# Kernel tuning notes

Measured on AMD Instinct MI355X. Metric: run time of the kernel, lower is better.

## Reference

```python
import jax, jax.numpy as jnp
import numpy as np

B, H = 1024, 256
HP = H // 2  # hyperparams_dim
W_SCALE = 0.08  # kaiming-uniform-like magnitude to keep tanh unsaturated


def setup_inputs() -> dict:
    key = jax.random.key(0)
    ks = jax.random.split(key, 8)
    return {
        "h_0": jax.random.normal(ks[0], (B, 1, H), dtype=jnp.float32),
        "h_t": jax.random.normal(ks[1], (B, 1, H), dtype=jnp.float32),
        "msg": jax.random.normal(ks[2], (B, 1, H), dtype=jnp.float32),
        "c": jax.random.uniform(ks[3], (1,), dtype=jnp.float32),
        "fc1_w": jax.random.normal(ks[4], (HP, H), dtype=jnp.float32) * W_SCALE,
        "fc2_w": jax.random.normal(ks[5], (HP, HP), dtype=jnp.float32) * W_SCALE,
        "fc3_w": jax.random.normal(ks[6], (HP, HP), dtype=jnp.float32) * W_SCALE,
        "fc4_w": jax.random.normal(ks[7], (2 * H * H, HP), dtype=jnp.float32) * W_SCALE,
    }


def reference(h_0, h_t, msg, c, fc1_w, fc2_w, fc3_w, fc4_w):
    # torch code clamps self.c into [0, 1] before use
    cc = jnp.clip(c, 0.0, 1.0)
    h = cc * h_0 + (1.0 - cc) * h_t                     # [B, 1, H]
    x = jnp.tanh(jnp.einsum('bsh,ph->bsp', h, fc1_w))    # [B, 1, HP]
    x = jnp.tanh(jnp.einsum('bsp,qp->bsq', x, fc2_w))    # [B, 1, HP]
    x = jnp.tanh(jnp.einsum('bsq,rq->bsr', x, fc3_w))    # [B, 1, HP]
    f4 = jnp.einsum('bsr,wr->bsw', x, fc4_w)             # [B, 1, 2*H*H]
    g1 = f4[..., : H * H].reshape(-1, H, H)              # [B, H, H]
    g2 = f4[..., H * H :].reshape(-1, H, H)              # [B, H, H]
    # F.linear(msg[i], g) == msg[i] @ g.T, batched over B
    g1_out = jnp.tanh(jnp.einsum('bsh,bkh->bsk', msg, g1))  # [B, 1, H]
    out = jnp.einsum('bsk,bok->bso', g1_out, g2)             # [B, 1, H]
    return out
```

## Files before the change

kernel.cpp:

```cpp
#include <hip/hip_runtime.h>
#include <hip/hip_bf16.h>

#define HDIM 256
#define HPDIM 128

typedef short bf8 __attribute__((ext_vector_type(8)));
typedef float f32x4 __attribute__((ext_vector_type(4)));

__device__ inline unsigned pkbf2(float a, float b) {
  float2 f; f.x = a; f.y = b;
  __hip_bfloat162 h = __float22bfloat162_rn(f);
  unsigned u; __builtin_memcpy(&u, &h, 4); return u;
}
__device__ inline unsigned short bfbits(float v) {
  __hip_bfloat16 h = __float2bfloat16(v);
  unsigned short u; __builtin_memcpy(&u, &h, 2); return u;
}
__device__ inline uint4 pack8u(float4 a, float4 b) {
  uint4 r;
  r.x = pkbf2(a.x, a.y); r.y = pkbf2(a.z, a.w);
  r.z = pkbf2(b.x, b.y); r.w = pkbf2(b.z, b.w);
  return r;
}
__device__ inline float fast_tanh(float x) {
  float t = __expf(2.0f * x);
  return 1.0f - 2.0f * __builtin_amdgcn_rcpf(t + 1.0f);
}
__device__ inline bf8 wfrag(const float* __restrict__ s) {
  float4 a = *(const float4*)s, b = *(const float4*)(s + 4);
  uint4 u = pack8u(a, b);
  bf8 r; __builtin_memcpy(&r, &u, 16); return r;
}

typedef const __attribute__((address_space(1))) unsigned int* gas_ptr;
typedef __attribute__((address_space(3))) unsigned int* las_ptr;
__device__ inline void gld_lds16(const void* g, void* l) {
  __builtin_amdgcn_global_load_lds((gas_ptr)g, (las_ptr)l, 16, 0, 0);
}

__global__ __launch_bounds__(256) void k_prep(
    const float* __restrict__ h0, const float* __restrict__ htv,
    const float* __restrict__ cp,
    const float* __restrict__ w1, const float* __restrict__ w2,
    const float* __restrict__ w3, const float* __restrict__ msg,
    const float* __restrict__ fc4,
    short* __restrict__ x3f, float* __restrict__ msgTT,
    short* __restrict__ fc4f) {
  const int t = threadIdx.x;
  const int bx = blockIdx.x;

  if (bx >= 80) {
    const int tile = bx - 80;
    const float* srcp = fc4 + (size_t)tile * (64 * 128);
    char* dstp = (char*)fc4f + (size_t)tile * (64 * 256);
    #pragma unroll
    for (int it = 0; it < 4; ++it) {
      int cid = it * 256 + t;
      int rl = cid >> 4, c = cid & 15;
      const float* s = srcp + rl * 128 + c * 8;
      float4 a = *(const float4*)s, b = *(const float4*)(s + 4);
      *(uint4*)(dstp + rl * 256 + ((c ^ (rl & 7)) << 4)) = pack8u(a, b);
    }
    return;
  }

  if (bx >= 64) {
    const int b0 = (bx - 64) * 64;
    #pragma unroll
    for (int it = 0; it < 16; ++it) {
      int u = it * 256 + t;
      int bl = u & 63, g = u >> 6;
      float4 v = *(const float4*)(msg + (size_t)(b0 + bl) * HDIM + g * 4);
      *(float4*)(msgTT + (size_t)g * 4096 + (b0 + bl) * 4) = v;
    }
    return;
  }

  __shared__ char hbuf[8192];
  __shared__ char xa[4096];
  __shared__ char xb[4096];
  const int wave = t >> 6, lane = t & 63;
  const int r16 = lane & 15, quad = lane >> 4;
  const int b0 = bx * 16;
  const float cc = fminf(fmaxf(cp[0], 0.f), 1.f);

  #pragma unroll
  for (int it = 0; it < 2; ++it) {
    int flat = it * 2048 + t * 8;
    int row = flat >> 8, col = flat & 255, kb = col >> 3;
    int gi = (b0 + row) * HDIM + col;
    float4 a = *(const float4*)(h0 + gi);
    float4 b = *(const float4*)(htv + gi);
    float4 va, vb;
    va.x = cc*a.x + (1.f-cc)*b.x; va.y = cc*a.y + (1.f-cc)*b.y;
    va.z = cc*a.z + (1.f-cc)*b.z; va.w = cc*a.w + (1.f-cc)*b.w;
    a = *(const float4*)(h0 + gi + 4); b = *(const float4*)(htv + gi + 4);
    vb.x = cc*a.x + (1.f-cc)*b.x; vb.y = cc*a.y + (1.f-cc)*b.y;
    vb.z = cc*a.z + (1.f-cc)*b.z; vb.w = cc*a.w + (1.f-cc)*b.w;
    *(uint4*)(hbuf + row*512 + ((kb ^ (row & 7)) << 4)) = pack8u(va, vb);
  }
  __syncthreads();

  {
    f32x4 acc[2] = {};
    #pragma unroll
    for (int ks = 0; ks < 8; ++ks) {
      bf8 af = *(bf8*)(hbuf + r16*512 + (((ks*4 + quad) ^ (r16 & 7)) << 4));
      #pragma unroll
      for (int nt = 0; nt < 2; ++nt) {
        bf8 bw_ = wfrag(w1 + ((wave*2 + nt)*16 + r16) * 256 + ks*32 + quad*8);
        acc[nt] = __builtin_amdgcn_mfma_f32_16x16x32_bf16(af, bw_, acc[nt], 0, 0, 0);
      }
    }
    #pragma unroll
    for (int nt = 0; nt < 2; ++nt)
      #pragma unroll
      for (int i = 0; i < 4; ++i) {
        int row = quad*4 + i, col = wave*32 + nt*16 + r16;
        *(unsigned short*)(xa + row*256 + (((col >> 3) ^ (row & 7)) << 4) + ((col & 7) << 1))
            = bfbits(fast_tanh(acc[nt][i]));
      }
  }
  __syncthreads();
  {
    f32x4 acc[2] = {};
    #pragma unroll
    for (int ks = 0; ks < 4; ++ks) {
      bf8 af = *(bf8*)(xa + r16*256 + (((ks*4 + quad) ^ (r16 & 7)) << 4));
      #pragma unroll
      for (int nt = 0; nt < 2; ++nt) {
        bf8 bw_ = wfrag(w2 + ((wave*2 + nt)*16 + r16) * 128 + ks*32 + quad*8);
        acc[nt] = __builtin_amdgcn_mfma_f32_16x16x32_bf16(af, bw_, acc[nt], 0, 0, 0);
      }
    }
    #pragma unroll
    for (int nt = 0; nt < 2; ++nt)
      #pragma unroll
      for (int i = 0; i < 4; ++i) {
        int row = quad*4 + i, col = wave*32 + nt*16 + r16;
        *(unsigned short*)(xb + row*256 + (((col >> 3) ^ (row & 7)) << 4) + ((col & 7) << 1))
            = bfbits(fast_tanh(acc[nt][i]));
      }
  }
  __syncthreads();
  {
    f32x4 acc[2] = {};
    #pragma unroll
    for (int ks = 0; ks < 4; ++ks) {
      bf8 af = *(bf8*)(xb + r16*256 + (((ks*4 + quad) ^ (r16 & 7)) << 4));
      #pragma unroll
      for (int nt = 0; nt < 2; ++nt) {
        bf8 bw_ = wfrag(w3 + ((wave*2 + nt)*16 + r16) * 128 + ks*32 + quad*8);
        acc[nt] = __builtin_amdgcn_mfma_f32_16x16x32_bf16(af, bw_, acc[nt], 0, 0, 0);
      }
    }
    #pragma unroll
    for (int nt = 0; nt < 2; ++nt)
      #pragma unroll
      for (int i = 0; i < 4; ++i) {
        int row = quad*4 + i, col = wave*32 + nt*16 + r16;
        *(unsigned short*)(xa + row*256 + (((col >> 3) ^ (row & 7)) << 4) + ((col & 7) << 1))
            = bfbits(fast_tanh(acc[nt][i]));
      }
  }
  __syncthreads();
  {
    int ks = t >> 6, l = t & 63, q2 = l >> 4, rr = l & 15;
    uint4 d = *(uint4*)(xa + rr*256 + (((ks*4 + q2) ^ (rr & 7)) << 4));
    *(uint4*)(x3f + (size_t)((bx*4 + ks)*64 + l)*8) = d;
  }
}

template<int PHASE>
__global__ __launch_bounds__(256, 3) void k_hyper(
    const short* __restrict__ x3f, const float* __restrict__ wTT,
    const short* __restrict__ fc4f, float* __restrict__ outp) {
  __shared__ char lds[2 * 16384];
  const int bxs = blockIdx.x;
  const int kcol = ((bxs & 7) << 5) | (bxs >> 3);
  const int t = threadIdx.x, wave = t >> 6, lane = t & 63;
  const int r16 = lane & 15, quad = lane >> 4;
  const int bw = blockIdx.y * 256 + wave * 64;

  bf8 xf[4][4];
  #pragma unroll
  for (int nt = 0; nt < 4; ++nt)
    #pragma unroll
    for (int ks = 0; ks < 4; ++ks)
      xf[nt][ks] = *(const bf8*)(x3f +
          (size_t)(((blockIdx.y*16 + wave*4 + nt)*4 + ks)*64 + lane)*8);

  const char* src = (const char*)fc4f +
      ((size_t)(PHASE ? 65536 : 0) + (size_t)kcol * 256) * 256;

  #pragma unroll
  for (int it = 0; it < 4; ++it)
    gld_lds16(src + it*4096 + t*16, (char*)lds + it*4096 + t*16);
  __syncthreads();

  float gacc[4] = {0.f, 0.f, 0.f, 0.f};
  const float* wbase = wTT + (size_t)quad * 4096 + (bw + r16) * 4;

  #pragma unroll 1
  for (int q = 0; q < 4; ++q) {
    char* buf = (char*)lds + (q & 1) * 16384;
    float4 wv[4];
    #pragma unroll
    for (int nt = 0; nt < 4; ++nt)
      wv[nt] = *(const float4*)(wbase + (size_t)(q * 16) * 4096 + nt * 64);
    if (q < 3) {
      char* nbuf = (char*)lds + ((q + 1) & 1) * 16384;
      const char* nsrc = src + (q + 1) * 16384;
      #pragma unroll
      for (int it = 0; it < 4; ++it)
        gld_lds16(nsrc + it*4096 + t*16, nbuf + it*4096 + t*16);
    }
    #pragma unroll
    for (int htl = 0; htl < 4; ++htl) {
      if (htl > 0) {
        #pragma unroll
        for (int nt = 0; nt < 4; ++nt)
          wv[nt] = *(const float4*)(wbase + (size_t)(q*16 + htl*4) * 4096 + nt * 64);
      }
      const int row = htl * 16 + r16;
      bf8 af[4];
      #pragma unroll
      for (int ks = 0; ks < 4; ++ks)
        af[ks] = *(bf8*)(buf + row*256 + (((ks*4 + quad) ^ (row & 7)) << 4));
      #pragma unroll
      for (int nt = 0; nt < 4; ++nt) {
        f32x4 acc = {};
        #pragma unroll
        for (int ks = 0; ks < 4; ++ks)
          acc = __builtin_amdgcn_mfma_f32_16x16x32_bf16(af[ks], xf[nt][ks], acc, 0, 0, 0);
        gacc[nt] += acc[0]*wv[nt].x + acc[1]*wv[nt].y + acc[2]*wv[nt].z + acc[3]*wv[nt].w;
      }
    }
    __syncthreads();
  }

  #pragma unroll
  for (int nt = 0; nt < 4; ++nt) {
    float v = gacc[nt];
    v += __shfl_xor(v, 16);
    v += __shfl_xor(v, 32);
    if (quad == 0) {
      int b = bw + nt*16 + r16;
      if (PHASE == 0) outp[(size_t)(kcol >> 2)*4096 + b*4 + (kcol & 3)] = fast_tanh(v);
      else            outp[b*HDIM + kcol] = v;
    }
  }
}

extern "C" void kernel_launch(void* const* d_in, const int* in_sizes, int n_in,
                              void* d_out, int out_size, void* d_ws, size_t ws_size,
                              hipStream_t stream) {
  const float* h0  = (const float*)d_in[0];
  const float* htt = (const float*)d_in[1];
  const float* msg = (const float*)d_in[2];
  const float* c   = (const float*)d_in[3];
  const float* w1  = (const float*)d_in[4];
  const float* w2  = (const float*)d_in[5];
  const float* w3  = (const float*)d_in[6];
  const float* w4  = (const float*)d_in[7];
  float* out = (float*)d_out;

  short* x3f  = (short*)d_ws;
  float* g1TT = (float*)((char*)d_ws + 262144);
  float* msgTT= (float*)((char*)d_ws + 262144 + 1048576);
  short* fc4f = (short*)((char*)d_ws + 262144 + 2097152);

  k_prep<<<dim3(2128), dim3(256), 0, stream>>>(h0, htt, c, w1, w2, w3, msg, w4,
                                               x3f, msgTT, fc4f);
  k_hyper<0><<<dim3(256, 4), dim3(256), 0, stream>>>(x3f, msgTT, fc4f, g1TT);
  k_hyper<1><<<dim3(256, 4), dim3(256), 0, stream>>>(x3f, g1TT, fc4f, out);
}
```

Before: 178.6 us.

## Convert fc4 to bf16 inside hyper kernels and load full tile into LDS

Removes the separate fp32-to-bf16 conversion pass over fc4 in k_prep. Each k_hyper block now reads its 256-row fc4 slice directly as fp32, converts it and stores the whole 64KB swizzled tile in LDS at once, replacing the double-buffered global_load_lds pipeline. Blocks grow to 512 threads covering 512 batch rows, so each fc4 slice is read by half as many blocks. The inner loop is unrolled with ping-pong register prefetch of LDS fragments and weights. The cost is that each phase now reads the fp32 weight twice from HBM and gets lower occupancy because of the 64KB LDS per block.

```diff
diff --git a/kernel.cpp b/kernel.cpp
--- a/kernel.cpp
+++ b/kernel.cpp
@@ -32,37 +32,14 @@
   bf8 r; __builtin_memcpy(&r, &u, 16); return r;
 }
 
-typedef const __attribute__((address_space(1))) unsigned int* gas_ptr;
-typedef __attribute__((address_space(3))) unsigned int* las_ptr;
-__device__ inline void gld_lds16(const void* g, void* l) {
-  __builtin_amdgcn_global_load_lds((gas_ptr)g, (las_ptr)l, 16, 0, 0);
-}
-
 __global__ __launch_bounds__(256) void k_prep(
     const float* __restrict__ h0, const float* __restrict__ htv,
     const float* __restrict__ cp,
     const float* __restrict__ w1, const float* __restrict__ w2,
     const float* __restrict__ w3, const float* __restrict__ msg,
-    const float* __restrict__ fc4,
-    short* __restrict__ x3f, float* __restrict__ msgTT,
-    short* __restrict__ fc4f) {
+    short* __restrict__ x3f, float* __restrict__ msgTT) {
   const int t = threadIdx.x;
   const int bx = blockIdx.x;
-
-  if (bx >= 80) {
-    const int tile = bx - 80;
-    const float* srcp = fc4 + (size_t)tile * (64 * 128);
-    char* dstp = (char*)fc4f + (size_t)tile * (64 * 256);
-    #pragma unroll
-    for (int it = 0; it < 4; ++it) {
-      int cid = it * 256 + t;
-      int rl = cid >> 4, c = cid & 15;
-      const float* s = srcp + rl * 128 + c * 8;
-      float4 a = *(const float4*)s, b = *(const float4*)(s + 4);
-      *(uint4*)(dstp + rl * 256 + ((c ^ (rl & 7)) << 4)) = pack8u(a, b);
-    }
-    return;
-  }
 
   if (bx >= 64) {
     const int b0 = (bx - 64) * 64;
@@ -172,15 +149,15 @@
 }
 
 template<int PHASE>
-__global__ __launch_bounds__(256, 3) void k_hyper(
+__global__ __launch_bounds__(512) void k_hyper(
     const short* __restrict__ x3f, const float* __restrict__ wTT,
-    const short* __restrict__ fc4f, float* __restrict__ outp) {
-  __shared__ char lds[2 * 16384];
+    const float* __restrict__ fc4, float* __restrict__ outp) {
+  __shared__ char lds[65536];
   const int bxs = blockIdx.x;
   const int kcol = ((bxs & 7) << 5) | (bxs >> 3);
   const int t = threadIdx.x, wave = t >> 6, lane = t & 63;
   const int r16 = lane & 15, quad = lane >> 4;
-  const int bw = blockIdx.y * 256 + wave * 64;
+  const int bw = blockIdx.y * 512 + wave * 64;
 
   bf8 xf[4][4];
   #pragma unroll
@@ -188,55 +165,68 @@
     #pragma unroll
     for (int ks = 0; ks < 4; ++ks)
       xf[nt][ks] = *(const bf8*)(x3f +
-          (size_t)(((blockIdx.y*16 + wave*4 + nt)*4 + ks)*64 + lane)*8);
-
-  const char* src = (const char*)fc4f +
-      ((size_t)(PHASE ? 65536 : 0) + (size_t)kcol * 256) * 256;
-
-  #pragma unroll
-  for (int it = 0; it < 4; ++it)
-    gld_lds16(src + it*4096 + t*16, (char*)lds + it*4096 + t*16);
+          (size_t)((((blockIdx.y*8 + wave)*4 + nt)*4 + ks)*64 + lane)*8);
+
+  const float* src = fc4 + ((size_t)(PHASE ? 65536 : 0) + (size_t)kcol * 256) * HPDIM;
+  #pragma unroll
+  for (int it = 0; it < 8; ++it) {
+    int cidx = it * 512 + t;
+    int row = cidx >> 4, kb = cidx & 15;
+    const float* s = src + cidx * 8;
+    float4 a = *(const float4*)s, b = *(const float4*)(s + 4);
+    *(uint4*)(lds + row*256 + ((kb ^ (row & 7)) << 4)) = pack8u(a, b);
+  }
   __syncthreads();
 
   float gacc[4] = {0.f, 0.f, 0.f, 0.f};
   const float* wbase = wTT + (size_t)quad * 4096 + (bw + r16) * 4;
 
-  #pragma unroll 1
-  for (int q = 0; q < 4; ++q) {
-    char* buf = (char*)lds + (q & 1) * 16384;
-    float4 wv[4];
-    #pragma unroll
-    for (int nt = 0; nt < 4; ++nt)
-      wv[nt] = *(const float4*)(wbase + (size_t)(q * 16) * 4096 + nt * 64);
-    if (q < 3) {
-      char* nbuf = (char*)lds + ((q + 1) & 1) * 16384;
-      const char* nsrc = src + (q + 1) * 16384;
-      #pragma unroll
-      for (int it = 0; it < 4; ++it)
-        gld_lds16(nsrc + it*4096 + t*16, nbuf + it*4096 + t*16);
-    }
-    #pragma unroll
-    for (int htl = 0; htl < 4; ++htl) {
-      if (htl > 0) {
-        #pragma unroll
-        for (int nt = 0; nt < 4; ++nt)
-          wv[nt] = *(const float4*)(wbase + (size_t)(q*16 + htl*4) * 4096 + nt * 64);
-      }
-      const int row = htl * 16 + r16;
-      bf8 af[4];
-      #pragma unroll
-      for (int ks = 0; ks < 4; ++ks)
-        af[ks] = *(bf8*)(buf + row*256 + (((ks*4 + quad) ^ (row & 7)) << 4));
-      #pragma unroll
-      for (int nt = 0; nt < 4; ++nt) {
-        f32x4 acc = {};
-        #pragma unroll
-        for (int ks = 0; ks < 4; ++ks)
-          acc = __builtin_amdgcn_mfma_f32_16x16x32_bf16(af[ks], xf[nt][ks], acc, 0, 0, 0);
-        gacc[nt] += acc[0]*wv[nt].x + acc[1]*wv[nt].y + acc[2]*wv[nt].z + acc[3]*wv[nt].w;
-      }
-    }
-    __syncthreads();
+  float4 wvA[4], wvB[4];
+  bf8 afA[4], afB[4];
+  #pragma unroll
+  for (int nt = 0; nt < 4; ++nt) wvA[nt] = *(const float4*)(wbase + nt * 64);
+  #pragma unroll
+  for (int ks = 0; ks < 4; ++ks)
+    afA[ks] = *(bf8*)(lds + r16*256 + (((ks*4 + quad) ^ (r16 & 7)) << 4));
+
+  #pragma unroll
+  for (int hp = 0; hp < 8; ++hp) {
+    const int hgB = hp*2 + 1;
+    {
+      const int row = hgB*16 + r16;
+      #pragma unroll
+      for (int nt = 0; nt < 4; ++nt)
+        wvB[nt] = *(const float4*)(wbase + (size_t)hgB*16384 + nt*64);
+      #pragma unroll
+      for (int ks = 0; ks < 4; ++ks)
+        afB[ks] = *(bf8*)(lds + row*256 + (((ks*4 + quad) ^ (row & 7)) << 4));
+    }
+    #pragma unroll
+    for (int nt = 0; nt < 4; ++nt) {
+      f32x4 acc = {};
+      #pragma unroll
+      for (int ks = 0; ks < 4; ++ks)
+        acc = __builtin_amdgcn_mfma_f32_16x16x32_bf16(afA[ks], xf[nt][ks], acc, 0, 0, 0);
+      gacc[nt] += acc[0]*wvA[nt].x + acc[1]*wvA[nt].y + acc[2]*wvA[nt].z + acc[3]*wvA[nt].w;
+    }
+    if (hp < 7) {
+      const int hgN = hp*2 + 2;
+      const int row = hgN*16 + r16;
+      #pragma unroll
+      for (int nt = 0; nt < 4; ++nt)
+        wvA[nt] = *(const float4*)(wbase + (size_t)hgN*16384 + nt*64);
+      #pragma unroll
+      for (int ks = 0; ks < 4; ++ks)
+        afA[ks] = *(bf8*)(lds + row*256 + (((ks*4 + quad) ^ (row & 7)) << 4));
+    }
+    #pragma unroll
+    for (int nt = 0; nt < 4; ++nt) {
+      f32x4 acc = {};
+      #pragma unroll
+      for (int ks = 0; ks < 4; ++ks)
+        acc = __builtin_amdgcn_mfma_f32_16x16x32_bf16(afB[ks], xf[nt][ks], acc, 0, 0, 0);
+      gacc[nt] += acc[0]*wvB[nt].x + acc[1]*wvB[nt].y + acc[2]*wvB[nt].z + acc[3]*wvB[nt].w;
+    }
   }
 
   #pragma unroll
@@ -268,10 +258,9 @@
   short* x3f  = (short*)d_ws;
   float* g1TT = (float*)((char*)d_ws + 262144);
   float* msgTT= (float*)((char*)d_ws + 262144 + 1048576);
-  short* fc4f = (short*)((char*)d_ws + 262144 + 2097152);
-
-  k_prep<<<dim3(2128), dim3(256), 0, stream>>>(h0, htt, c, w1, w2, w3, msg, w4,
-                                               x3f, msgTT, fc4f);
-  k_hyper<0><<<dim3(256, 4), dim3(256), 0, stream>>>(x3f, msgTT, fc4f, g1TT);
-  k_hyper<1><<<dim3(256, 4), dim3(256), 0, stream>>>(x3f, g1TT, fc4f, out);
-}
+
+  k_prep<<<dim3(80), dim3(256), 0, stream>>>(h0, htt, c, w1, w2, w3, msg,
+                                             x3f, msgTT);
+  k_hyper<0><<<dim3(256, 2), dim3(512), 0, stream>>>(x3f, msgTT, w4, g1TT);
+  k_hyper<1><<<dim3(256, 2), dim3(512), 0, stream>>>(x3f, g1TT, w4, out);
+}
```

New measurement: 455.4 us. 2.55x slower.
